# Kernel optimization log

Measured on AMD Instinct MI355X. Metric: run time of the kernel, lower is better.

## Reference

```python
import jax, jax.numpy as jnp
import numpy as np


def setup_inputs() -> dict:
    key = jax.random.key(0)
    ks = jax.random.split(key, 4)
    B, C, H, W = 8, 64, 256, 256
    return {
        "x": jax.random.normal(ks[0], (B, C, H, W), jnp.float32),
        "fc_w": jax.random.normal(ks[1], (C, C), jnp.float32) / np.sqrt(C).astype(np.float32),
        "fc_b": jnp.zeros((C,), jnp.float32),
        "conv1_w": jax.random.normal(ks[2], (2,), jnp.float32),  # [mean_ch, max_ch] of 1x1 conv
        "conv1_b": jnp.zeros((1,), jnp.float32),
        "conv2_w": jax.random.normal(ks[3], (2,), jnp.float32),
        "conv2_b": jnp.zeros((1,), jnp.float32),
        "size": 4,
    }


def reference(x, fc_w, fc_b, conv1_w, conv1_b, conv2_w, conv2_b, size):
    B, C, H, W = x.shape
    s = size
    h, w = H // s, W // s
    # unfold (non-overlapping) -> [B, L, C, s*s], L = h*w, patch pixels row-major
    p = x.reshape(B, C, h, s, w, s).transpose(0, 2, 4, 1, 3, 5).reshape(B, h * w, C, s * s)
    # channel attention: max over patch pixels -> fc -> sigmoid
    m = jax.nn.sigmoid(jnp.max(p, axis=3) @ fc_w.T + fc_b)  # [B, L, C]
    p = p * m[..., None]
    # spatial-in-patch attention: (mean, max) over channel axis -> 1x1 conv(2->1) -> sigmoid
    g1 = jax.nn.sigmoid(
        conv1_w[0] * jnp.mean(p, axis=2, keepdims=True)
        + conv1_w[1] * jnp.max(p, axis=2, keepdims=True)
        + conv1_b[0]
    )  # [B, L, 1, s*s]
    p = p * g1
    # fold back to [B, C, H, W]
    y = p.reshape(B, h, w, C, s, s).transpose(0, 3, 1, 4, 2, 5).reshape(B, C, H, W)
    # per-patch gating: (mean, max) over all C*s*s values of each patch
    yb = y.reshape(B, C, h, s, w, s)
    mx = jnp.max(yb, axis=(1, 3, 5))   # [B, h, w]
    mn = jnp.mean(yb, axis=(1, 3, 5))  # [B, h, w]
    g2 = jax.nn.sigmoid(conv2_w[0] * mn + conv2_w[1] * mx + conv2_b[0])
    g2 = jnp.repeat(jnp.repeat(g2, s, axis=1), s, axis=2)  # [B, H, W]
    return y * g2[:, None, :, :]
```

## Files before the change

kernel.cpp:

```cpp
#include <hip/hip_runtime.h>
#include <math.h>

constexpr int Bc = 8, Cc = 64, Hc = 256, Wc = 256, Sc = 4;
constexpr int NPATCH = Bc * (Hc / Sc) * (Wc / Sc);
constexpr int TP = 8;
constexpr int CPITCH = 133;
constexpr int RPITCH = 33;

__device__ __forceinline__ float sigmoidf_(float v) {
    return 1.0f / (1.0f + __expf(-v));
}

__global__ __launch_bounds__(256, 2)
void ciam_kernel(const float* __restrict__ x,
                 const float* __restrict__ fc_w,
                 const float* __restrict__ fc_b,
                 const float* __restrict__ c1w,
                 const float* __restrict__ c1b,
                 const float* __restrict__ c2w,
                 const float* __restrict__ c2b,
                 float* __restrict__ out)
{
    __shared__ float T[64 * CPITCH];
    __shared__ float fcw_lds[64 * 65];
    __shared__ float maxbuf[TP][64];
    __shared__ float pixbuf[4][16 * 65];
    __shared__ float g1buf[4][2][16];

    const int tid  = threadIdx.x;
    const int gid  = blockIdx.x;
    const int b    = gid >> 9;
    const int rem  = gid & 511;
    const int ph   = rem >> 3;
    const int pwg  = rem & 7;
    const int col0 = pwg * 32;

    #pragma unroll
    for (int i = 0; i < 4; ++i) {
        int u   = i * 256 + tid;
        int row = u >> 4;
        int jf  = (u & 15) << 2;
        const float4 wv = *reinterpret_cast<const float4*>(fc_w + row * 64 + jf);
        float* fd = &fcw_lds[row * 65 + jf];
        fd[0] = wv.x; fd[1] = wv.y; fd[2] = wv.z; fd[3] = wv.w;
    }

    #pragma unroll
    for (int i = 0; i < 8; ++i) {
        int u   = i * 256 + tid;
        int seg = u >> 3;
        int c_  = seg >> 2;
        int r_  = seg & 3;
        int j4  = (u & 7) << 2;
        const float4 val = *reinterpret_cast<const float4*>(
            x + (((size_t)(b * Cc + c_) * Hc + (ph * Sc + r_)) * Wc + col0 + j4));
        float* td = &T[c_ * CPITCH + r_ * RPITCH + j4];
        td[0] = val.x; td[1] = val.y; td[2] = val.z; td[3] = val.w;
    }

    const float w10 = c1w[0], w11 = c1w[1], b1 = c1b[0];
    const float w20 = c2w[0], w21 = c2w[1], b2 = c2b[0];

    __syncthreads();

    const int wave = tid >> 6;
    const int lane = tid & 63;
    const int c    = lane;
    const int p0   = wave * 2;

    float v[2][16];
    #pragma unroll
    for (int pi = 0; pi < 2; ++pi) {
        const float* tp = &T[c * CPITCH + (p0 + pi) * 4];
        #pragma unroll
        for (int r = 0; r < 4; ++r)
            #pragma unroll
            for (int j = 0; j < 4; ++j)
                v[pi][r * 4 + j] = tp[r * RPITCH + j];
    }

    float mx0 = -3.4e38f, mx1 = -3.4e38f;
    #pragma unroll
    for (int t = 0; t < 16; ++t) {
        mx0 = fmaxf(mx0, v[0][t]);
        mx1 = fmaxf(mx1, v[1][t]);
    }
    maxbuf[p0][c]     = mx0;
    maxbuf[p0 + 1][c] = mx1;
    __syncthreads();

    float a0 = fc_b[c], a1 = a0;
    #pragma unroll 16
    for (int k = 0; k < 64; ++k) {
        float wv = fcw_lds[c * 65 + k];
        a0 = fmaf(wv, maxbuf[p0][k], a0);
        a1 = fmaf(wv, maxbuf[p0 + 1][k], a1);
    }
    const float m0 = sigmoidf_(a0), m1 = sigmoidf_(a1);
    #pragma unroll
    for (int t = 0; t < 16; ++t) { v[0][t] *= m0; v[1][t] *= m1; }

    #pragma unroll
    for (int pi = 0; pi < 2; ++pi) {
        #pragma unroll
        for (int t = 0; t < 16; ++t)
            pixbuf[wave][t * 65 + c] = v[pi][t];
        __syncthreads();
        {
            const int a = lane >> 2, q = lane & 3;
            const float* pb = &pixbuf[wave][a * 65 + q * 16];
            float s = 0.f, mxp = -3.4e38f;
            #pragma unroll
            for (int t = 0; t < 16; ++t) {
                float u = pb[t];
                s += u;
                mxp = fmaxf(mxp, u);
            }
            s   += __shfl_xor(s, 1);
            s   += __shfl_xor(s, 2);
            mxp  = fmaxf(mxp, __shfl_xor(mxp, 1));
            mxp  = fmaxf(mxp, __shfl_xor(mxp, 2));
            float g1 = sigmoidf_(w10 * (s * (1.f / 64.f)) + w11 * mxp + b1);
            if (q == 0) g1buf[wave][pi][a] = g1;
        }
        __syncthreads();
        #pragma unroll
        for (int t = 0; t < 16; ++t)
            v[pi][t] *= g1buf[wave][pi][t];
    }

    #pragma unroll
    for (int pi = 0; pi < 2; ++pi) {
        float ls = 0.f, lmx = -3.4e38f;
        #pragma unroll
        for (int t = 0; t < 16; ++t) {
            ls += v[pi][t];
            lmx = fmaxf(lmx, v[pi][t]);
        }
        #pragma unroll
        for (int off = 32; off >= 1; off >>= 1) {
            ls  += __shfl_xor(ls, off);
            lmx  = fmaxf(lmx, __shfl_xor(lmx, off));
        }
        const float g2 = sigmoidf_(w20 * (ls * (1.f / 1024.f)) + w21 * lmx + b2);
        float* tp = &T[c * CPITCH + (p0 + pi) * 4];
        #pragma unroll
        for (int r = 0; r < 4; ++r)
            #pragma unroll
            for (int j = 0; j < 4; ++j)
                tp[r * RPITCH + j] = v[pi][r * 4 + j] * g2;
    }
    __syncthreads();

    #pragma unroll
    for (int i = 0; i < 8; ++i) {
        int u   = i * 256 + tid;
        int seg = u >> 3;
        int c_  = seg >> 2;
        int r_  = seg & 3;
        int j4  = (u & 7) << 2;
        const float* ts = &T[c_ * CPITCH + r_ * RPITCH + j4];
        float4 o;
        o.x = ts[0]; o.y = ts[1]; o.z = ts[2]; o.w = ts[3];
        *reinterpret_cast<float4*>(
            out + (((size_t)(b * Cc + c_) * Hc + (ph * Sc + r_)) * Wc + col0 + j4)) = o;
    }
}

extern "C" void kernel_launch(void* const* d_in, const int* in_sizes, int n_in,
                              void* d_out, int out_size, void* d_ws, size_t ws_size,
                              hipStream_t stream) {
    const float* x    = (const float*)d_in[0];
    const float* fc_w = (const float*)d_in[1];
    const float* fc_b = (const float*)d_in[2];
    const float* c1w  = (const float*)d_in[3];
    const float* c1b  = (const float*)d_in[4];
    const float* c2w  = (const float*)d_in[5];
    const float* c2b  = (const float*)d_in[6];

    float* out = (float*)d_out;
    ciam_kernel<<<NPATCH / TP, 256, 0, stream>>>(x, fc_w, fc_b, c1w, c1b, c2w, c2b, out);
}
```

Baseline: 258.2 us.

## Factor patch gates algebraically and store tile in patch-major float4 layout

The LDS tile now stores each patch's 16 pixels contiguously per channel, so loads and stores can use float4. The per-pixel register array is gone. Channel, pixel and patch gates are computed from LDS and written as small scale buffers. The patch mean and max are derived algebraically from g1 times the per-pixel channel sum and max, which holds because g1 is positive. The final output pass applies all three gates in one multiply, and occupancy is raised to 3 blocks per CU, aiming to cut register pressure, LDS traffic and one barrier round-trip.

Measured after the change: 261.0 us. Within noise of the previous version (+1.1%).

```diff
diff --git a/kernel.cpp b/kernel.cpp
--- a/kernel.cpp
+++ b/kernel.cpp
@@ -4,14 +4,15 @@
 constexpr int Bc = 8, Cc = 64, Hc = 256, Wc = 256, Sc = 4;
 constexpr int NPATCH = Bc * (Hc / Sc) * (Wc / Sc);
 constexpr int TP = 8;
-constexpr int CPITCH = 133;
-constexpr int RPITCH = 33;
+constexpr int CP = 132;
+constexpr int MP = 65;
+constexpr int GP = 20;
 
 __device__ __forceinline__ float sigmoidf_(float v) {
     return 1.0f / (1.0f + __expf(-v));
 }
 
-__global__ __launch_bounds__(256, 2)
+__global__ __launch_bounds__(256, 3)
 void ciam_kernel(const float* __restrict__ x,
                  const float* __restrict__ fc_w,
                  const float* __restrict__ fc_b,
@@ -21,19 +22,18 @@
                  const float* __restrict__ c2b,
                  float* __restrict__ out)
 {
-    __shared__ float T[64 * CPITCH];
-    __shared__ float fcw_lds[64 * 65];
-    __shared__ float maxbuf[TP][64];
-    __shared__ float pixbuf[4][16 * 65];
-    __shared__ float g1buf[4][2][16];
+    __shared__ float T[64 * CP];
+    __shared__ float fcw[64 * 65];
+    __shared__ float cmbuf[TP * MP];
+    __shared__ float g1buf[TP * GP];
+    __shared__ float g2buf[TP];
 
-    const int tid  = threadIdx.x;
-    const int gid  = blockIdx.x;
+    const int tid = threadIdx.x;
+    const int gid = blockIdx.x;
     const int b    = gid >> 9;
     const int rem  = gid & 511;
     const int ph   = rem >> 3;
-    const int pwg  = rem & 7;
-    const int col0 = pwg * 32;
+    const int col0 = (rem & 7) * 32;
 
     #pragma unroll
     for (int i = 0; i < 4; ++i) {
@@ -41,7 +41,7 @@
         int row = u >> 4;
         int jf  = (u & 15) << 2;
         const float4 wv = *reinterpret_cast<const float4*>(fc_w + row * 64 + jf);
-        float* fd = &fcw_lds[row * 65 + jf];
+        float* fd = &fcw[row * 65 + jf];
         fd[0] = wv.x; fd[1] = wv.y; fd[2] = wv.z; fd[3] = wv.w;
     }
 
@@ -51,11 +51,10 @@
         int seg = u >> 3;
         int c_  = seg >> 2;
         int r_  = seg & 3;
-        int j4  = (u & 7) << 2;
+        int p_  = u & 7;
         const float4 val = *reinterpret_cast<const float4*>(
-            x + (((size_t)(b * Cc + c_) * Hc + (ph * Sc + r_)) * Wc + col0 + j4));
-        float* td = &T[c_ * CPITCH + r_ * RPITCH + j4];
-        td[0] = val.x; td[1] = val.y; td[2] = val.z; td[3] = val.w;
+            x + (((size_t)(b * Cc + c_) * Hc + (ph * Sc + r_)) * Wc + col0 + 4 * p_));
+        *reinterpret_cast<float4*>(&T[c_ * CP + p_ * 16 + r_ * 4]) = val;
     }
 
     const float w10 = c1w[0], w11 = c1w[1], b1 = c1b[0];
@@ -65,90 +64,70 @@
 
     const int wave = tid >> 6;
     const int lane = tid & 63;
-    const int c    = lane;
     const int p0   = wave * 2;
-
-    float v[2][16];
-    #pragma unroll
-    for (int pi = 0; pi < 2; ++pi) {
-        const float* tp = &T[c * CPITCH + (p0 + pi) * 4];
-        #pragma unroll
-        for (int r = 0; r < 4; ++r)
-            #pragma unroll
-            for (int j = 0; j < 4; ++j)
-                v[pi][r * 4 + j] = tp[r * RPITCH + j];
-    }
-
-    float mx0 = -3.4e38f, mx1 = -3.4e38f;
-    #pragma unroll
-    for (int t = 0; t < 16; ++t) {
-        mx0 = fmaxf(mx0, v[0][t]);
-        mx1 = fmaxf(mx1, v[1][t]);
-    }
-    maxbuf[p0][c]     = mx0;
-    maxbuf[p0 + 1][c] = mx1;
-    __syncthreads();
-
-    float a0 = fc_b[c], a1 = a0;
-    #pragma unroll 16
-    for (int k = 0; k < 64; ++k) {
-        float wv = fcw_lds[c * 65 + k];
-        a0 = fmaf(wv, maxbuf[p0][k], a0);
-        a1 = fmaf(wv, maxbuf[p0 + 1][k], a1);
-    }
-    const float m0 = sigmoidf_(a0), m1 = sigmoidf_(a1);
-    #pragma unroll
-    for (int t = 0; t < 16; ++t) { v[0][t] *= m0; v[1][t] *= m1; }
 
     #pragma unroll
     for (int pi = 0; pi < 2; ++pi) {
+        const float* tp = &T[lane * CP + (p0 + pi) * 16];
+        float4 a = *reinterpret_cast<const float4*>(tp + 0);
+        float4 bq = *reinterpret_cast<const float4*>(tp + 4);
+        float4 cq = *reinterpret_cast<const float4*>(tp + 8);
+        float4 dq = *reinterpret_cast<const float4*>(tp + 12);
+        float mv = fmaxf(fmaxf(fmaxf(a.x, a.y), fmaxf(a.z, a.w)),
+                         fmaxf(fmaxf(bq.x, bq.y), fmaxf(bq.z, bq.w)));
+        mv = fmaxf(mv, fmaxf(fmaxf(cq.x, cq.y), fmaxf(cq.z, cq.w)));
+        mv = fmaxf(mv, fmaxf(fmaxf(dq.x, dq.y), fmaxf(dq.z, dq.w)));
+        cmbuf[(p0 + pi) * MP + lane] = mv;
+    }
+    __syncthreads();
+
+    {
+        const float bias = fc_b[lane];
+        float a0 = bias, a1 = bias;
+        const float* m0p = &cmbuf[p0 * MP];
+        const float* m1p = &cmbuf[(p0 + 1) * MP];
+        const float* wr  = &fcw[lane * 65];
+        #pragma unroll 16
+        for (int k = 0; k < 64; ++k) {
+            float wv = wr[k];
+            a0 = fmaf(wv, m0p[k], a0);
+            a1 = fmaf(wv, m1p[k], a1);
+        }
+        float m0 = sigmoidf_(a0), m1 = sigmoidf_(a1);
+        cmbuf[p0 * MP + lane]       = m0;
+        cmbuf[(p0 + 1) * MP + lane] = m1;
+    }
+    __syncthreads();
+
+    {
+        const int q = lane >> 4, t = lane & 15;
         #pragma unroll
-        for (int t = 0; t < 16; ++t)
-            pixbuf[wave][t * 65 + c] = v[pi][t];
-        __syncthreads();
-        {
-            const int a = lane >> 2, q = lane & 3;
-            const float* pb = &pixbuf[wave][a * 65 + q * 16];
-            float s = 0.f, mxp = -3.4e38f;
+        for (int pi = 0; pi < 2; ++pi) {
+            const int p = p0 + pi;
+            const float* tp = &T[(q * 16) * CP + p * 16 + t];
+            const float* mp = &cmbuf[p * MP + q * 16];
+            float s = 0.f, mx = -3.4e38f;
             #pragma unroll
-            for (int t = 0; t < 16; ++t) {
-                float u = pb[t];
+            for (int i = 0; i < 16; ++i) {
+                float u = tp[i * CP] * mp[i];
                 s += u;
-                mxp = fmaxf(mxp, u);
+                mx = fmaxf(mx, u);
             }
-            s   += __shfl_xor(s, 1);
-            s   += __shfl_xor(s, 2);
-            mxp  = fmaxf(mxp, __shfl_xor(mxp, 1));
-            mxp  = fmaxf(mxp, __shfl_xor(mxp, 2));
-            float g1 = sigmoidf_(w10 * (s * (1.f / 64.f)) + w11 * mxp + b1);
-            if (q == 0) g1buf[wave][pi][a] = g1;
+            s  += __shfl_xor(s, 16);
+            s  += __shfl_xor(s, 32);
+            mx  = fmaxf(mx, __shfl_xor(mx, 16));
+            mx  = fmaxf(mx, __shfl_xor(mx, 32));
+            const float g1 = sigmoidf_(w10 * (s * (1.f / 64.f)) + w11 * mx + b1);
+            float pa = g1 * s, pm = g1 * mx;
+            #pragma unroll
+            for (int off = 1; off <= 8; off <<= 1) {
+                pa += __shfl_xor(pa, off);
+                pm  = fmaxf(pm, __shfl_xor(pm, off));
+            }
+            const float g2 = sigmoidf_(w20 * (pa * (1.f / 1024.f)) + w21 * pm + b2);
+            if (lane < 16) g1buf[p * GP + lane] = g1;
+            if (lane == 0) g2buf[p] = g2;
         }
-        __syncthreads();
-        #pragma unroll
-        for (int t = 0; t < 16; ++t)
-            v[pi][t] *= g1buf[wave][pi][t];
-    }
-
-    #pragma unroll
-    for (int pi = 0; pi < 2; ++pi) {
-        float ls = 0.f, lmx = -3.4e38f;
-        #pragma unroll
-        for (int t = 0; t < 16; ++t) {
-            ls += v[pi][t];
-            lmx = fmaxf(lmx, v[pi][t]);
-        }
-        #pragma unroll
-        for (int off = 32; off >= 1; off >>= 1) {
-            ls  += __shfl_xor(ls, off);
-            lmx  = fmaxf(lmx, __shfl_xor(lmx, off));
-        }
-        const float g2 = sigmoidf_(w20 * (ls * (1.f / 1024.f)) + w21 * lmx + b2);
-        float* tp = &T[c * CPITCH + (p0 + pi) * 4];
-        #pragma unroll
-        for (int r = 0; r < 4; ++r)
-            #pragma unroll
-            for (int j = 0; j < 4; ++j)
-                tp[r * RPITCH + j] = v[pi][r * 4 + j] * g2;
     }
     __syncthreads();
 
@@ -158,12 +137,17 @@
         int seg = u >> 3;
         int c_  = seg >> 2;
         int r_  = seg & 3;
-        int j4  = (u & 7) << 2;
-        const float* ts = &T[c_ * CPITCH + r_ * RPITCH + j4];
+        int p_  = u & 7;
+        const float4 xv = *reinterpret_cast<const float4*>(&T[c_ * CP + p_ * 16 + r_ * 4]);
+        const float ms = cmbuf[p_ * MP + c_] * g2buf[p_];
+        const float4 g1v = *reinterpret_cast<const float4*>(&g1buf[p_ * GP + r_ * 4]);
         float4 o;
-        o.x = ts[0]; o.y = ts[1]; o.z = ts[2]; o.w = ts[3];
+        o.x = xv.x * ms * g1v.x;
+        o.y = xv.y * ms * g1v.y;
+        o.z = xv.z * ms * g1v.z;
+        o.w = xv.w * ms * g1v.w;
         *reinterpret_cast<float4*>(
-            out + (((size_t)(b * Cc + c_) * Hc + (ph * Sc + r_)) * Wc + col0 + j4)) = o;
+            out + (((size_t)(b * Cc + c_) * Hc + (ph * Sc + r_)) * Wc + col0 + 4 * p_)) = o;
     }
 }
 
```
